# Performance work log

Hardware: AMD Instinct MI355X
Metric: run time of the kernel (lower is better)

## Reference

```python
import jax, jax.numpy as jnp
import numpy as np

B, S, V = 512, 256, 10      # batch, s_node_num, v_node_num
E, H = 128, 128             # embedding, lstm hidden
D = 2 * H                   # num_directions * hidden
PENALTY = 1.0e6
STD = 0.1


def _cell(x, h, c, Wih, Whh, b):
    # PyTorch LSTM cell, gate order i, f, g, o; b = b_ih + b_hh
    g = x @ Wih.T + h @ Whh.T + b
    i, f, gg, o = jnp.split(g, 4, axis=-1)
    c = jax.nn.sigmoid(f) * c + jax.nn.sigmoid(i) * jnp.tanh(gg)
    h = jax.nn.sigmoid(o) * jnp.tanh(c)
    return h, c


def setup_inputs() -> dict:
    key = jax.random.key(0)
    ks = jax.random.split(key, 25)
    w = lambda k, shp: (jax.random.normal(k, shp, jnp.float32) * STD)
    return {
        's_node_indexes': jax.random.randint(ks[0], (B, S), 0, S, dtype=jnp.int32),
        's_inputs': jax.random.uniform(ks[1], (B, S, 3), jnp.float32),
        'v_input': jax.random.uniform(ks[2], (V, 3), jnp.float32) * 0.5,
        'W_embed': w(ks[3], (E, 1)),
        'enc_Wih_f': w(ks[4], (4 * H, E)), 'enc_Whh_f': w(ks[5], (4 * H, H)), 'enc_b_f': w(ks[6], (4 * H,)),
        'enc_Wih_b': w(ks[7], (4 * H, E)), 'enc_Whh_b': w(ks[8], (4 * H, H)), 'enc_b_b': w(ks[9], (4 * H,)),
        'dec_Wih_f': w(ks[10], (4 * H, D)), 'dec_Whh_f': w(ks[11], (4 * H, H)), 'dec_b_f': w(ks[12], (4 * H,)),
        'dec_Wih_b': w(ks[13], (4 * H, D)), 'dec_Whh_b': w(ks[14], (4 * H, H)), 'dec_b_b': w(ks[15], (4 * H,)),
        'W_ref': w(ks[16], (D, D)), 'W_q': w(ks[17], (D, D)), 'v_w': w(ks[18], (D,)),
        'W_ref2': w(ks[19], (D, D)), 'W_q2': w(ks[20], (D, D)), 'v2_w': w(ks[21], (D,)),
    }


def reference(s_node_indexes, s_inputs, v_input, W_embed,
              enc_Wih_f, enc_Whh_f, enc_b_f, enc_Wih_b, enc_Whh_b, enc_b_b,
              dec_Wih_f, dec_Whh_f, dec_b_f, dec_Wih_b, dec_Whh_b, dec_b_b,
              W_ref, W_q, v_w, W_ref2, W_q2, v2_w):
    Bn, Sn = s_node_indexes.shape
    # Embed: snode resource -> Linear(1, E, bias=False)
    emb = s_inputs[:, :, 0:1] @ W_embed.T            # (B, S, E)
    xs = jnp.swapaxes(emb, 0, 1)                     # (S, B, E)
    h0 = jnp.zeros((Bn, H), jnp.float32)
    c0 = jnp.zeros((Bn, H), jnp.float32)

    def enc_scan(Wih, Whh, b, seq):
        def step(carry, x):
            h, c = carry
            h, c = _cell(x, h, c, Wih, Whh, b)
            return (h, c), h
        (hT, cT), hs = jax.lax.scan(step, (h0, c0), seq)
        return hs, hT, cT

    hs_f, hf, cf = enc_scan(enc_Wih_f, enc_Whh_f, enc_b_f, xs)
    hs_b, hb, cb = enc_scan(enc_Wih_b, enc_Whh_b, enc_b_b, xs[::-1])
    Enc = jnp.swapaxes(jnp.concatenate([hs_f, hs_b[::-1]], axis=-1), 0, 1)  # (B, S, D)
    h_state = jnp.stack([hf, hb])                    # (2, B, H)
    c_state = jnp.stack([cf, cb])

    refE = Enc @ W_ref.T                             # (B, S, D) precomputed (dropout p=0)
    ref2E = Enc @ W_ref2.T

    def dec_step(carry, vcpu):
        dec_in, h, c, played = carry                 # dec_in (B, D)
        hf_, cf_ = _cell(dec_in, h[0], c[0], dec_Wih_f, dec_Whh_f, dec_b_f)
        hb_, cb_ = _cell(dec_in, h[1], c[1], dec_Wih_b, dec_Whh_b, dec_b_b)
        dec_out = jnp.concatenate([hf_, hb_], axis=-1)                       # (B, D)
        cannot = (s_inputs[:, :, 0] < vcpu).astype(jnp.float32) + played     # (B, S)
        ow = jnp.tanh(refE + (dec_out @ W_q.T)[:, None, :]) @ v_w - PENALTY * cannot
        att = jax.nn.softmax(jnp.tanh(ref2E + (dec_in @ W_q2.T)[:, None, :]) @ v2_w, axis=1)
        new_in = jnp.einsum('bs,bsd->bd', att, Enc)
        sel = jnp.argmax(ow, axis=1)
        played = played + jax.nn.one_hot(sel, Sn, dtype=jnp.float32)
        return (new_in, jnp.stack([hf_, hb_]), jnp.stack([cf_, cb_]), played), (ow, sel)

    init = (jnp.zeros((Bn, D), jnp.float32), h_state, c_state, jnp.zeros((Bn, Sn), jnp.float32))
    _, (output_weights, sels) = jax.lax.scan(dec_step, init, v_input[:, 0])
    shuffled = sels.T                                # (B, V)
    original = jnp.take_along_axis(s_node_indexes, shuffled, axis=1)
    return original, shuffled, output_weights        # output_weights: (V, B, S)
```

## Files before the change

kernel.cpp:

```cpp
#include <hip/hip_runtime.h>
#include <math.h>

#define cB 512
#define cS 256
#define cV 10
#define cE 128
#define cH 128
#define cD 256
#define cG 512
#define PEN 1.0e6f
#define PADK 40
#define S1OW 112
#define L1OW 144
#define S2AT 128
#define L2AT 128

typedef _Float16 half8_t __attribute__((ext_vector_type(8)));
typedef _Float16 half4_t __attribute__((ext_vector_type(4)));
typedef float f32x4 __attribute__((ext_vector_type(4)));

#define DOT4(acc, wv, hv)                                   \
    do {                                                    \
        acc = fmaf((wv).x, (hv).x, acc);                    \
        acc = fmaf((wv).y, (hv).y, acc);                    \
        acc = fmaf((wv).z, (hv).z, acc);                    \
        acc = fmaf((wv).w, (hv).w, acc);                    \
    } while (0)

__device__ __forceinline__ float sigmf(float x) { return 1.0f / (1.0f + expf(-x)); }

__global__ void k_uprep(const float* __restrict__ Wih_f, const float* __restrict__ Wih_b,
                        const float* __restrict__ W_embed, float* __restrict__ uvec)
{
    const int j = threadIdx.x;
    const float* __restrict__ Wih = blockIdx.x ? Wih_b : Wih_f;
    float u = 0.f;
#pragma unroll 8
    for (int e = 0; e < cE; ++e) u = fmaf(Wih[(size_t)j * cE + e], W_embed[e], u);
    uvec[blockIdx.x * cG + j] = u;
}

__global__ __launch_bounds__(1024, 4) void k_encoder(
    const float* __restrict__ s_inputs, const float* __restrict__ uvec,
    const float* __restrict__ Whh_f, const float* __restrict__ b_f,
    const float* __restrict__ Whh_b, const float* __restrict__ b_b,
    _Float16* __restrict__ Ehi, _Float16* __restrict__ Elo,
    float* __restrict__ h_state, float* __restrict__ c_state)
{
    const int dir = blockIdx.x >> 7;
    const int b0  = (blockIdx.x & 127) * 4;
    const float* __restrict__ Whh = dir ? Whh_b : Whh_f;
    const float* __restrict__ bv  = dir ? b_b   : b_f;
    const int tid = threadIdx.x;
    const int j = tid & 511;
    const int hf = tid >> 9;

    __shared__ __align__(16) float a_in[4][cS];
    __shared__ __align__(16) float hbuf[4][cH];
    __shared__ __align__(16) float gpart[4][2][516];

    a_in[tid >> 8][tid & 255] =
        s_inputs[((size_t)(b0 + (tid >> 8)) * cS + (tid & 255)) * 3];

    float4 w[16];
#pragma unroll
    for (int kk = 0; kk < 16; ++kk)
        w[kk] = *(const float4*)&Whh[(size_t)j * cH + hf * 64 + kk * 4];

    const float uj = (hf == 0) ? uvec[dir * cG + j] : 0.f;
    const float bj = (hf == 0) ? bv[j] : 0.f;

    const int ur = tid >> 7, uk = tid & 127;
    float c_reg = 0.f, h_last = 0.f;
    if (tid < 512) hbuf[ur][uk] = 0.f;
    __syncthreads();

    for (int p = 0; p < cS; ++p) {
        const int s = dir ? (cS - 1 - p) : p;
        float a0[4];
#pragma unroll
        for (int r = 0; r < 4; ++r) a0[r] = fmaf(a_in[r][s], uj, bj);
#pragma unroll
        for (int kk = 0; kk < 16; ++kk) {
            const float4 wv = w[kk];
#pragma unroll
            for (int r = 0; r < 4; ++r) {
                const float4 h4 = *(const float4*)&hbuf[r][hf * 64 + kk * 4];
                DOT4(a0[r], wv, h4);
            }
        }
#pragma unroll
        for (int r = 0; r < 4; ++r) gpart[r][hf][j] = a0[r];
        __syncthreads();

        if (tid < 512) {
            const float gi = gpart[ur][0][uk]       + gpart[ur][1][uk];
            const float gf = gpart[ur][0][128 + uk] + gpart[ur][1][128 + uk];
            const float gg = gpart[ur][0][256 + uk] + gpart[ur][1][256 + uk];
            const float go = gpart[ur][0][384 + uk] + gpart[ur][1][384 + uk];
            const float i_ = sigmf(gi), f_ = sigmf(gf), g_ = tanhf(gg), o_ = sigmf(go);
            c_reg = fmaf(f_, c_reg, i_ * g_);
            const float hn = o_ * tanhf(c_reg);
            h_last = hn;
            hbuf[ur][uk] = hn;
            const size_t eidx = ((size_t)(b0 + ur) * cS + s) * cD + dir * cH + uk;
            const _Float16 hh = (_Float16)hn;
            Ehi[eidx] = hh;
            Elo[eidx] = (_Float16)(hn - (float)hh);
        }
        __syncthreads();
    }
    if (tid < 512) {
        h_state[((size_t)dir * cB + b0 + ur) * cH + uk] = h_last;
        c_state[((size_t)dir * cB + b0 + ur) * cH + uk] = c_reg;
    }
}

__global__ void k_split_w(const float* __restrict__ W1, const float* __restrict__ W2,
                          _Float16* __restrict__ Whi1, _Float16* __restrict__ Wlo1,
                          _Float16* __restrict__ Whi2, _Float16* __restrict__ Wlo2)
{
    const int i = blockIdx.x * 256 + threadIdx.x;
    {
        float a = W1[i]; _Float16 h = (_Float16)a;
        Whi1[i] = h; Wlo1[i] = (_Float16)(a - (float)h);
    }
    {
        float a = W2[i]; _Float16 h = (_Float16)a;
        Whi2[i] = h; Wlo2[i] = (_Float16)(a - (float)h);
    }
}

__global__ __launch_bounds__(256) void k_head_mat2(
    const _Float16* __restrict__ Ahi, const _Float16* __restrict__ Alo,
    const _Float16* __restrict__ Whi1, const _Float16* __restrict__ Wlo1,
    const _Float16* __restrict__ Whi2, const _Float16* __restrict__ Wlo2,
    float* __restrict__ refC, float* __restrict__ ref2C)
{
    const int blk = blockIdx.x;
    const bool is1 = blk < (S1OW * cB / 64);
    const _Float16* __restrict__ Whi = is1 ? Whi1 : Whi2;
    const _Float16* __restrict__ Wlo = is1 ? Wlo1 : Wlo2;
    float* __restrict__ outv = is1 ? refC : ref2C;
    const int m0 = (is1 ? blk : blk - S1OW * cB / 64) * 64;

    const int tid = threadIdx.x;
    const int w = tid >> 6, l = tid & 63;

    __shared__ __align__(16) _Float16 As[2][64][PADK];
    __shared__ __align__(16) _Float16 Ws[2][256][PADK];

    const int r = tid >> 2, kq = tid & 3;
    size_t arow;
    {
        const int m = m0 + r;
        const int s = m >> 9, b = m & 511;
        arow = ((size_t)b * cS + s) * cD;
    }
    const size_t wrow = (size_t)tid * cD;

    f32x4 acc[16];
#pragma unroll
    for (int i = 0; i < 16; ++i) acc[i] = (f32x4){0.f, 0.f, 0.f, 0.f};

    const int fr = w * 16 + (l & 15);
    const int kc = (l >> 4) * 8;

    for (int k0 = 0; k0 < 256; k0 += 32) {
        __syncthreads();
        *(uint4*)&As[0][r][kq * 8] = *(const uint4*)&Ahi[arow + k0 + kq * 8];
        *(uint4*)&As[1][r][kq * 8] = *(const uint4*)&Alo[arow + k0 + kq * 8];
#pragma unroll
        for (int q4 = 0; q4 < 4; ++q4) {
            *(uint4*)&Ws[0][tid][q4 * 8] = *(const uint4*)&Whi[wrow + k0 + q4 * 8];
            *(uint4*)&Ws[1][tid][q4 * 8] = *(const uint4*)&Wlo[wrow + k0 + q4 * 8];
        }
        __syncthreads();

        const half8_t ahi = *(const half8_t*)&As[0][fr][kc];
        const half8_t alo = *(const half8_t*)&As[1][fr][kc];
#pragma unroll
        for (int nf = 0; nf < 16; ++nf) {
            const int n = nf * 16 + (l & 15);
            const half8_t bhi = *(const half8_t*)&Ws[0][n][kc];
            const half8_t blo = *(const half8_t*)&Ws[1][n][kc];
            acc[nf] = __builtin_amdgcn_mfma_f32_16x16x32_f16(ahi, bhi, acc[nf], 0, 0, 0);
            acc[nf] = __builtin_amdgcn_mfma_f32_16x16x32_f16(ahi, blo, acc[nf], 0, 0, 0);
            acc[nf] = __builtin_amdgcn_mfma_f32_16x16x32_f16(alo, bhi, acc[nf], 0, 0, 0);
        }
    }
#pragma unroll
    for (int nf = 0; nf < 16; ++nf)
#pragma unroll
        for (int rr = 0; rr < 4; ++rr) {
            const int m = w * 16 + ((l >> 4) << 2) + rr;
            outv[(size_t)(m0 + m) * cD + nf * 16 + (l & 15)] = acc[nf][rr];
        }
}

__global__ __launch_bounds__(512, 2) void k_score(
    const _Float16* __restrict__ Ahi, const _Float16* __restrict__ Alo,
    const _Float16* __restrict__ Whi1, const _Float16* __restrict__ Wlo1,
    const _Float16* __restrict__ Whi2, const _Float16* __restrict__ Wlo2,
    const float* __restrict__ refC, const float* __restrict__ ref2C,
    const float* __restrict__ q1v, const float* __restrict__ q2v,
    const float* __restrict__ v_w, const float* __restrict__ v2_w,
    float* __restrict__ sc1lo, float* __restrict__ sc1hi,
    float* __restrict__ sc2lo, float* __restrict__ sc2hi)
{
    __shared__ __align__(16) char smem[65536];
    const int blk = blockIdx.x;
    const int tid = threadIdx.x;

    if (blk < 1088) {
        const bool isow = blk < 576;
        const _Float16* __restrict__ Whi = isow ? Whi1 : Whi2;
        const _Float16* __restrict__ Wlo = isow ? Wlo1 : Wlo2;
        const int batt = blk - 576;
        const int m0 = isow ? blk * 128 : 0;

        _Float16 (*Ah)[PADK] = (_Float16(*)[PADK])(smem);
        _Float16 (*Al)[PADK] = (_Float16(*)[PADK])(smem + 10240);
        _Float16 (*Wh)[PADK] = (_Float16(*)[PADK])(smem + 20480);
        _Float16 (*Wl)[PADK] = (_Float16(*)[PADK])(smem + 40960);
        float* qs = (float*)(smem + 61440);
        float* vs = (float*)(smem + 62464);
        float (*spart)[128] = (float(*)[128])(smem + 63488);

        const int l = tid & 63;
        const int w = tid >> 6;
        const int wm = w >> 2, wn = w & 3;
        const int g = l >> 4, li = l & 15;

        if (isow) {
            if (tid < 256) vs[tid] = v_w[tid];
        } else {
            if (tid < 256) qs[tid] = q2v[(size_t)batt * cD + tid];
            else           vs[tid - 256] = v2_w[tid - 256];
        }

        const int ar = tid >> 2, aq = tid & 3;
        size_t arow;
        if (isow) {
            const int m = m0 + ar;
            const int bq = m / L1OW;
            const int s = S1OW + (m - bq * L1OW);
            arow = ((size_t)bq * cS + s) * cD;
        } else {
            arow = ((size_t)batt * cS + S2AT + ar) * cD;
        }

        f32x4 acc[4][4];
#pragma unroll
        for (int mi = 0; mi < 4; ++mi)
#pragma unroll
            for (int ni = 0; ni < 4; ++ni) acc[mi][ni] = (f32x4){0.f, 0.f, 0.f, 0.f};

        for (int k0 = 0; k0 < 256; k0 += 32) {
            __syncthreads();
            *(uint4*)&Ah[ar][aq * 8] = *(const uint4*)&Ahi[arow + k0 + aq * 8];
            *(uint4*)&Al[ar][aq * 8] = *(const uint4*)&Alo[arow + k0 + aq * 8];
            *(uint4*)&Wh[ar][aq * 8] = *(const uint4*)&Whi[(size_t)ar * cD + k0 + aq * 8];
            *(uint4*)&Wl[ar][aq * 8] = *(const uint4*)&Wlo[(size_t)ar * cD + k0 + aq * 8];
            *(uint4*)&Wh[ar + 128][aq * 8] = *(const uint4*)&Whi[(size_t)(ar + 128) * cD + k0 + aq * 8];
            *(uint4*)&Wl[ar + 128][aq * 8] = *(const uint4*)&Wlo[(size_t)(ar + 128) * cD + k0 + aq * 8];
            __syncthreads();

            half8_t ah[4], al[4];
#pragma unroll
            for (int mi = 0; mi < 4; ++mi) {
                ah[mi] = *(const half8_t*)&Ah[wm * 64 + mi * 16 + li][g * 8];
                al[mi] = *(const half8_t*)&Al[wm * 64 + mi * 16 + li][g * 8];
            }
#pragma unroll
            for (int ni = 0; ni < 4; ++ni) {
                const half8_t bh = *(const half8_t*)&Wh[wn * 64 + ni * 16 + li][g * 8];
                const half8_t bl = *(const half8_t*)&Wl[wn * 64 + ni * 16 + li][g * 8];
#pragma unroll
                for (int mi = 0; mi < 4; ++mi) {
                    acc[mi][ni] = __builtin_amdgcn_mfma_f32_16x16x32_f16(ah[mi], bh, acc[mi][ni], 0, 0, 0);
                    acc[mi][ni] = __builtin_amdgcn_mfma_f32_16x16x32_f16(ah[mi], bl, acc[mi][ni], 0, 0, 0);
                    acc[mi][ni] = __builtin_amdgcn_mfma_f32_16x16x32_f16(al[mi], bh, acc[mi][ni], 0, 0, 0);
                }
            }
        }

        float val = 0.f;
#pragma unroll
        for (int mi = 0; mi < 4; ++mi)
#pragma unroll
            for (int rr = 0; rr < 4; ++rr) {
                const int row = wm * 64 + mi * 16 + g * 4 + rr;
                float p = 0.f;
#pragma unroll
                for (int ni = 0; ni < 4; ++ni) {
                    const int c = wn * 64 + ni * 16 + li;
                    const float qq = isow ? q1v[(size_t)((m0 + row) / L1OW) * cD + c]
                                          : qs[c];
                    p = fmaf(vs[c], tanhf(acc[mi][ni][rr] + qq), p);
                }
                p += __shfl_xor(p, 1);
                p += __shfl_xor(p, 2);
                p += __shfl_xor(p, 4);
                p += __shfl_xor(p, 8);
                if (li == mi * 4 + rr) val = p;
            }
        {
            const int row_out = wm * 64 + (li >> 2) * 16 + g * 4 + (li & 3);
            spart[wn][row_out] = val;
        }
        __syncthreads();
        if (tid < 128) {
            const float o = spart[0][tid] + spart[1][tid] + spart[2][tid] + spart[3][tid];
            if (isow) sc1hi[m0 + tid] = o;
            else      sc2hi[(size_t)batt * L2AT + tid] = o;
        }
    } else {
        const int fb = blk - 1088;
        const bool isowf = fb < 448;
        const float* __restrict__ C  = isowf ? refC : ref2C;
        const float* __restrict__ qv = isowf ? q1v : q2v;
        const float* __restrict__ vv = isowf ? v_w : v2_w;
        float* __restrict__ outv     = isowf ? sc1lo : sc2lo;
        const int m0 = (isowf ? fb : fb - 448) * 128;

        float (*red)[4] = (float(*)[4])smem;
        const int r = tid >> 2, p2 = tid & 3;
        const int m = m0 + r;
        const int b = m & 511;

        const float* row  = C + (size_t)m * cD + p2 * 64;
        const float* qrow = qv + (size_t)b * cD + p2 * 64;
        const float* vrow = vv + p2 * 64;
        float s = 0.f;
#pragma unroll 4
        for (int d = 0; d < 64; d += 4) {
            const float4 rv4 = *(const float4*)&row[d];
            const float4 q4  = *(const float4*)&qrow[d];
            const float4 v4  = *(const float4*)&vrow[d];
            s = fmaf(v4.x, tanhf(rv4.x + q4.x), s);
            s = fmaf(v4.y, tanhf(rv4.y + q4.y), s);
            s = fmaf(v4.z, tanhf(rv4.z + q4.z), s);
            s = fmaf(v4.w, tanhf(rv4.w + q4.w), s);
        }
        red[r][p2] = s;
        __syncthreads();
        if (tid < 128)
            outv[m0 + tid] = red[tid][0] + red[tid][1] + red[tid][2] + red[tid][3];
    }
}

__global__ __launch_bounds__(512, 2) void k_dec_cells(
    const float* __restrict__ dec_in,
    const float* __restrict__ Wih_f, const float* __restrict__ Whh_f, const float* __restrict__ b_f,
    const float* __restrict__ Wih_b, const float* __restrict__ Whh_b, const float* __restrict__ b_b,
    float* __restrict__ h_state, float* __restrict__ c_state, float* __restrict__ dec_out)
{
    const int cell = blockIdx.x >> 7;
    const int b0 = (blockIdx.x & 127) * 4;
    const float* __restrict__ Wih = cell ? Wih_b : Wih_f;
    const float* __restrict__ Whh = cell ? Whh_b : Whh_f;
    const float* __restrict__ bv  = cell ? b_b   : b_f;
    const int j = threadIdx.x;

    __shared__ __align__(16) float xin[4][cD];
    __shared__ __align__(16) float hin[4][cH];
    __shared__ __align__(16) float gbuf[4][cG];

    for (int idx = j; idx < 4 * cD; idx += 512) {
        int bb = idx >> 8, k = idx & 255;
        xin[bb][k] = dec_in[(size_t)(b0 + bb) * cD + k];
    }
    {
        int bb = j >> 7, k = j & 127;
        hin[bb][k] = h_state[((size_t)cell * cB + b0 + bb) * cH + k];
    }
    __syncthreads();

    float a0 = bv[j];
    float a1 = a0, a2 = a0, a3 = a0;
#pragma unroll 4
    for (int kk = 0; kk < 64; ++kk) {
        const float4 wv = *(const float4*)&Wih[(size_t)j * cD + kk * 4];
        const float4 x0 = *(const float4*)&xin[0][kk * 4]; DOT4(a0, wv, x0);
        const float4 x1 = *(const float4*)&xin[1][kk * 4]; DOT4(a1, wv, x1);
        const float4 x2 = *(const float4*)&xin[2][kk * 4]; DOT4(a2, wv, x2);
        const float4 x3 = *(const float4*)&xin[3][kk * 4]; DOT4(a3, wv, x3);
    }
#pragma unroll 4
    for (int kk = 0; kk < 32; ++kk) {
        const float4 wv = *(const float4*)&Whh[(size_t)j * cH + kk * 4];
        const float4 h0 = *(const float4*)&hin[0][kk * 4]; DOT4(a0, wv, h0);
        const float4 h1 = *(const float4*)&hin[1][kk * 4]; DOT4(a1, wv, h1);
        const float4 h2 = *(const float4*)&hin[2][kk * 4]; DOT4(a2, wv, h2);
        const float4 h3 = *(const float4*)&hin[3][kk * 4]; DOT4(a3, wv, h3);
    }
    gbuf[0][j] = a0; gbuf[1][j] = a1; gbuf[2][j] = a2; gbuf[3][j] = a3;
    __syncthreads();

    const int uk = j & 127, ub = j >> 7;
    const float gi = gbuf[ub][uk];
    const float gf = gbuf[ub][128 + uk];
    const float gg = gbuf[ub][256 + uk];
    const float go = gbuf[ub][384 + uk];
    const size_t sidx = ((size_t)cell * cB + b0 + ub) * cH + uk;
    const float c_old = c_state[sidx];
    const float i_ = sigmf(gi), f_ = sigmf(gf), g_ = tanhf(gg), o_ = sigmf(go);
    const float cn = fmaf(f_, c_old, i_ * g_);
    const float hn = o_ * tanhf(cn);
    c_state[sidx] = cn;
    h_state[sidx] = hn;
    dec_out[(size_t)(b0 + ub) * cD + cell * cH + uk] = hn;
}

__global__ __launch_bounds__(256, 2) void k_qproj(
    const float* __restrict__ dec_out, const float* __restrict__ dec_in_old,
    const float* __restrict__ W_q, const float* __restrict__ W_q2,
    float* __restrict__ q1v, float* __restrict__ q2v)
{
    const int b = blockIdx.x;
    const int tid = threadIdx.x;
    __shared__ __align__(16) float dout[cD];
    __shared__ __align__(16) float din[cD];
    dout[tid] = dec_out[(size_t)b * cD + tid];
    din[tid]  = dec_in_old[(size_t)b * cD + tid];
    __syncthreads();
    float s1 = 0.0f, s2 = 0.0f;
#pragma unroll 4
    for (int kk = 0; kk < 64; ++kk) {
        const float4 w1 = *(const float4*)&W_q[(size_t)tid * cD + kk * 4];
        const float4 w2 = *(const float4*)&W_q2[(size_t)tid * cD + kk * 4];
        const float4 x1 = *(const float4*)&dout[kk * 4];
        const float4 x2 = *(const float4*)&din[kk * 4];
        DOT4(s1, w1, x1);
        DOT4(s2, w2, x2);
    }
    q1v[(size_t)b * cD + tid] = s1;
    q2v[(size_t)b * cD + tid] = s2;
}

__global__ __launch_bounds__(256, 2) void k_finish(
    const float* __restrict__ sc1lo, const float* __restrict__ sc1hi,
    const float* __restrict__ sc2lo, const float* __restrict__ sc2hi,
    const _Float16* __restrict__ Ehi, const _Float16* __restrict__ Elo,
    const float* __restrict__ s_inputs, const int* __restrict__ s_node_indexes,
    const float* __restrict__ v_input, float* __restrict__ played,
    float* __restrict__ dec_in_new, float* __restrict__ outp, int t)
{
    const int b = blockIdx.x;
    const int tid = threadIdx.x;
    const int lane = tid & 63;
    const int wv = tid >> 6;

    __shared__ __align__(16) float atr[cS];
    __shared__ __align__(16) float part[4][cD];
    __shared__ float rv[cS];
    __shared__ int   ri[cS];

    const float owv = (tid < S1OW) ? sc1lo[(size_t)tid * cB + b]
                                   : sc1hi[(size_t)b * L1OW + (tid - S1OW)];
    atr[tid] = (tid < S2AT) ? sc2lo[(size_t)tid * cB + b]
                            : sc2hi[(size_t)b * L2AT + (tid - S2AT)];

    const float vcpu = v_input[t * 3];
    float val;
    {
        const float a0 = s_inputs[((size_t)b * cS + tid) * 3];
        const float can = (a0 < vcpu ? 1.0f : 0.0f) + played[(size_t)b * cS + tid];
        val = owv - PEN * can;
        outp[2 * cB * cV + ((size_t)t * cB + b) * cS + tid] = val;
    }
    rv[tid] = val; ri[tid] = tid;
    __syncthreads();
#pragma unroll
    for (int off = 128; off > 0; off >>= 1) {
        if (tid < off) {
            const float v2 = rv[tid + off]; const int i2 = ri[tid + off];
            const float v1 = rv[tid];       const int i1 = ri[tid];
            if (v2 > v1 || (v2 == v1 && i2 < i1)) { rv[tid] = v2; ri[tid] = i2; }
        }
        __syncthreads();
    }
    const int sel = ri[0];
    __syncthreads();
    if (tid == 0) {
        played[(size_t)b * cS + sel] += 1.0f;
        outp[(size_t)b * cV + t] = (float)s_node_indexes[(size_t)b * cS + sel];
        outp[(size_t)cB * cV + (size_t)b * cV + t] = (float)sel;
    }

    rv[tid] = atr[tid];
    __syncthreads();
#pragma unroll
    for (int off = 128; off > 0; off >>= 1) {
        if (tid < off) { const float v2 = rv[tid + off]; if (v2 > rv[tid]) rv[tid] = v2; }
        __syncthreads();
    }
    const float mx = rv[0];
    __syncthreads();
    const float ex = expf(atr[tid] - mx);
    rv[tid] = ex;
    __syncthreads();
#pragma unroll
    for (int off = 128; off > 0; off >>= 1) {
        if (tid < off) rv[tid] += rv[tid + off];
        __syncthreads();
    }
    const float ssum = rv[0];
    __syncthreads();
    atr[tid] = ex / ssum;
    __syncthreads();

    {
        float4 acc = make_float4(0.f, 0.f, 0.f, 0.f);
        for (int s2i = wv * 64; s2i < wv * 64 + 64; ++s2i) {
            const float a = atr[s2i];
            const size_t eidx = ((size_t)b * cS + s2i) * cD + lane * 4;
            const half4_t h4 = *(const half4_t*)&Ehi[eidx];
            const half4_t l4 = *(const half4_t*)&Elo[eidx];
            acc.x = fmaf(a, (float)h4[0] + (float)l4[0], acc.x);
            acc.y = fmaf(a, (float)h4[1] + (float)l4[1], acc.y);
            acc.z = fmaf(a, (float)h4[2] + (float)l4[2], acc.z);
            acc.w = fmaf(a, (float)h4[3] + (float)l4[3], acc.w);
        }
        *(float4*)&part[wv][lane * 4] = acc;
    }
    __syncthreads();
    dec_in_new[(size_t)b * cD + tid] =
        part[0][tid] + part[1][tid] + part[2][tid] + part[3][tid];
}

extern "C" void kernel_launch(void* const* d_in, const int* in_sizes, int n_in,
                              void* d_out, int out_size, void* d_ws, size_t ws_size,
                              hipStream_t stream)
{
    (void)in_sizes; (void)n_in; (void)out_size; (void)ws_size;

    const int*   s_node = (const int*)  d_in[0];
    const float* s_inp  = (const float*)d_in[1];
    const float* v_inp  = (const float*)d_in[2];
    const float* W_emb  = (const float*)d_in[3];
    const float* eWih_f = (const float*)d_in[4];
    const float* eWhh_f = (const float*)d_in[5];
    const float* eb_f   = (const float*)d_in[6];
    const float* eWih_b = (const float*)d_in[7];
    const float* eWhh_b = (const float*)d_in[8];
    const float* eb_b   = (const float*)d_in[9];
    const float* dWih_f = (const float*)d_in[10];
    const float* dWhh_f = (const float*)d_in[11];
    const float* db_f   = (const float*)d_in[12];
    const float* dWih_b = (const float*)d_in[13];
    const float* dWhh_b = (const float*)d_in[14];
    const float* db_b   = (const float*)d_in[15];
    const float* W_ref  = (const float*)d_in[16];
    const float* W_q    = (const float*)d_in[17];
    const float* v_w    = (const float*)d_in[18];
    const float* W_ref2 = (const float*)d_in[19];
    const float* W_q2   = (const float*)d_in[20];
    const float* v2_w   = (const float*)d_in[21];

    float* out = (float*)d_out;
    const size_t ENCSZ = (size_t)cB * cS * cD;
    const size_t SMALL = (size_t)cB * cD;

    char* p = (char*)d_ws;
    _Float16* Ehi  = (_Float16*)p; p += ENCSZ * 2;
    _Float16* Elo  = (_Float16*)p; p += ENCSZ * 2;
    float* refC    = (float*)p;    p += (size_t)S1OW * cB * cD * 4;
    float* ref2C   = (float*)p;    p += (size_t)S2AT * cB * cD * 4;
    _Float16* Whi1 = (_Float16*)p; p += (size_t)cD * cD * 2;
    _Float16* Wlo1 = (_Float16*)p; p += (size_t)cD * cD * 2;
    _Float16* Whi2 = (_Float16*)p; p += (size_t)cD * cD * 2;
    _Float16* Wlo2 = (_Float16*)p; p += (size_t)cD * cD * 2;
    float* hst    = (float*)p; p += SMALL * 4;
    float* cst    = (float*)p; p += SMALL * 4;
    float* din0   = (float*)p; p += SMALL * 4;
    float* din1   = (float*)p; p += SMALL * 4;
    float* doutb  = (float*)p; p += SMALL * 4;
    float* played = (float*)p; p += SMALL * 4;
    float* q1v    = (float*)p; p += SMALL * 4;
    float* q2v    = (float*)p; p += SMALL * 4;
    float* sc1lo  = (float*)p; p += (size_t)S1OW * cB * 4;
    float* sc1hi  = (float*)p; p += (size_t)L1OW * cB * 4;
    float* sc2lo  = (float*)p; p += (size_t)S2AT * cB * 4;
    float* sc2hi  = (float*)p; p += (size_t)L2AT * cB * 4;
    float* uvec   = (float*)p; p += 2 * cG * 4;

    hipMemsetAsync(played, 0, SMALL * sizeof(float), stream);
    hipMemsetAsync(din0,   0, SMALL * sizeof(float), stream);

    k_split_w<<<256, 256, 0, stream>>>(W_ref, W_ref2, Whi1, Wlo1, Whi2, Wlo2);
    k_uprep<<<2, 512, 0, stream>>>(eWih_f, eWih_b, W_emb, uvec);

    k_encoder<<<256, 1024, 0, stream>>>(s_inp, uvec, eWhh_f, eb_f, eWhh_b, eb_b,
                                        Ehi, Elo, hst, cst);

    k_head_mat2<<<(S1OW + S2AT) * cB / 64, 256, 0, stream>>>(
        Ehi, Elo, Whi1, Wlo1, Whi2, Wlo2, refC, ref2C);

    for (int t = 0; t < cV; ++t) {
        float* di_old = (t & 1) ? din1 : din0;
        float* di_new = (t & 1) ? din0 : din1;
        k_dec_cells<<<256, 512, 0, stream>>>(di_old, dWih_f, dWhh_f, db_f,
                                             dWih_b, dWhh_b, db_b, hst, cst, doutb);
        k_qproj<<<512, 256, 0, stream>>>(doutb, di_old, W_q, W_q2, q1v, q2v);
        k_score<<<2048, 512, 0, stream>>>(Ehi, Elo, Whi1, Wlo1, Whi2, Wlo2,
                                          refC, ref2C, q1v, q2v, v_w, v2_w,
                                          sc1lo, sc1hi, sc2lo, sc2hi);
        k_finish<<<512, 256, 0, stream>>>(sc1lo, sc1hi, sc2lo, sc2hi, Ehi, Elo,
                                          s_inp, s_node, v_inp, played, di_new, out, t);
    }
}
```

Before: 3.119 ms.

## Fuse both score heads into shared-A MFMA tiles and rebalance precompute split

The score kernel's on-the-fly MFMA path now computes both the output-weight and attention heads in one block, sharing the staged encoder A tile across two weight sets, with 256-thread blocks running two N passes. The split between precomputed ref projections and per-step recomputation is unified at one boundary (SCA/LST) for both heads, and the fallback path uses 64-row blocks. This aims to halve encoder tile loads per step and balance the grid. In exchange it adds accumulator register pressure, a larger shared buffer and more precomputed workspace.

```diff
diff --git a/kernel.cpp b/kernel.cpp
--- a/kernel.cpp
+++ b/kernel.cpp
@@ -10,10 +10,8 @@
 #define cG 512
 #define PEN 1.0e6f
 #define PADK 40
-#define S1OW 112
-#define L1OW 144
-#define S2AT 128
-#define L2AT 128
+#define SCA 120
+#define LST 136
 
 typedef _Float16 half8_t __attribute__((ext_vector_type(8)));
 typedef _Float16 half4_t __attribute__((ext_vector_type(4)));
@@ -138,11 +136,11 @@
     float* __restrict__ refC, float* __restrict__ ref2C)
 {
     const int blk = blockIdx.x;
-    const bool is1 = blk < (S1OW * cB / 64);
+    const bool is1 = blk < (SCA * cB / 64);
     const _Float16* __restrict__ Whi = is1 ? Whi1 : Whi2;
     const _Float16* __restrict__ Wlo = is1 ? Wlo1 : Wlo2;
     float* __restrict__ outv = is1 ? refC : ref2C;
-    const int m0 = (is1 ? blk : blk - S1OW * cB / 64) * 64;
+    const int m0 = (is1 ? blk : blk - SCA * cB / 64) * 64;
 
     const int tid = threadIdx.x;
     const int w = tid >> 6, l = tid & 63;
@@ -198,7 +196,7 @@
         }
 }
 
-__global__ __launch_bounds__(512, 2) void k_score(
+__global__ __launch_bounds__(256, 2) void k_score(
     const _Float16* __restrict__ Ahi, const _Float16* __restrict__ Alo,
     const _Float16* __restrict__ Whi1, const _Float16* __restrict__ Wlo1,
     const _Float16* __restrict__ Whi2, const _Float16* __restrict__ Wlo2,
@@ -208,121 +206,133 @@
     float* __restrict__ sc1lo, float* __restrict__ sc1hi,
     float* __restrict__ sc2lo, float* __restrict__ sc2hi)
 {
-    __shared__ __align__(16) char smem[65536];
+    __shared__ __align__(16) char smem[67584];
     const int blk = blockIdx.x;
     const int tid = threadIdx.x;
 
-    if (blk < 1088) {
-        const bool isow = blk < 576;
-        const _Float16* __restrict__ Whi = isow ? Whi1 : Whi2;
-        const _Float16* __restrict__ Wlo = isow ? Wlo1 : Wlo2;
-        const int batt = blk - 576;
-        const int m0 = isow ? blk * 128 : 0;
-
-        _Float16 (*Ah)[PADK] = (_Float16(*)[PADK])(smem);
-        _Float16 (*Al)[PADK] = (_Float16(*)[PADK])(smem + 10240);
-        _Float16 (*Wh)[PADK] = (_Float16(*)[PADK])(smem + 20480);
-        _Float16 (*Wl)[PADK] = (_Float16(*)[PADK])(smem + 40960);
-        float* qs = (float*)(smem + 61440);
-        float* vs = (float*)(smem + 62464);
-        float (*spart)[128] = (float(*)[128])(smem + 63488);
+    if (blk < 544) {
+        _Float16 (*Ah)[PADK]  = (_Float16(*)[PADK])(smem);
+        _Float16 (*Al)[PADK]  = (_Float16(*)[PADK])(smem + 10240);
+        _Float16 (*W1h)[PADK] = (_Float16(*)[PADK])(smem + 20480);
+        _Float16 (*W1l)[PADK] = (_Float16(*)[PADK])(smem + 30720);
+        _Float16 (*W2h)[PADK] = (_Float16(*)[PADK])(smem + 40960);
+        _Float16 (*W2l)[PADK] = (_Float16(*)[PADK])(smem + 51200);
+        float* vs1 = (float*)(smem + 61440);
+        float* vs2 = (float*)(smem + 62464);
+        float (*spart)[4][128] = (float(*)[4][128])(smem + 63488);
 
         const int l = tid & 63;
         const int w = tid >> 6;
-        const int wm = w >> 2, wn = w & 3;
+        const int wm = w >> 1, wn = w & 1;
         const int g = l >> 4, li = l & 15;
-
-        if (isow) {
-            if (tid < 256) vs[tid] = v_w[tid];
-        } else {
-            if (tid < 256) qs[tid] = q2v[(size_t)batt * cD + tid];
-            else           vs[tid - 256] = v2_w[tid - 256];
-        }
+        const int m0 = blk * 128;
+
+        vs1[tid] = v_w[tid];
+        vs2[tid] = v2_w[tid];
 
         const int ar = tid >> 2, aq = tid & 3;
-        size_t arow;
-        if (isow) {
-            const int m = m0 + ar;
-            const int bq = m / L1OW;
-            const int s = S1OW + (m - bq * L1OW);
-            arow = ((size_t)bq * cS + s) * cD;
-        } else {
-            arow = ((size_t)batt * cS + S2AT + ar) * cD;
-        }
-
-        f32x4 acc[4][4];
-#pragma unroll
-        for (int mi = 0; mi < 4; ++mi)
-#pragma unroll
-            for (int ni = 0; ni < 4; ++ni) acc[mi][ni] = (f32x4){0.f, 0.f, 0.f, 0.f};
-
-        for (int k0 = 0; k0 < 256; k0 += 32) {
-            __syncthreads();
-            *(uint4*)&Ah[ar][aq * 8] = *(const uint4*)&Ahi[arow + k0 + aq * 8];
-            *(uint4*)&Al[ar][aq * 8] = *(const uint4*)&Alo[arow + k0 + aq * 8];
-            *(uint4*)&Wh[ar][aq * 8] = *(const uint4*)&Whi[(size_t)ar * cD + k0 + aq * 8];
-            *(uint4*)&Wl[ar][aq * 8] = *(const uint4*)&Wlo[(size_t)ar * cD + k0 + aq * 8];
-            *(uint4*)&Wh[ar + 128][aq * 8] = *(const uint4*)&Whi[(size_t)(ar + 128) * cD + k0 + aq * 8];
-            *(uint4*)&Wl[ar + 128][aq * 8] = *(const uint4*)&Wlo[(size_t)(ar + 128) * cD + k0 + aq * 8];
-            __syncthreads();
-
-            half8_t ah[4], al[4];
-#pragma unroll
-            for (int mi = 0; mi < 4; ++mi) {
-                ah[mi] = *(const half8_t*)&Ah[wm * 64 + mi * 16 + li][g * 8];
-                al[mi] = *(const half8_t*)&Al[wm * 64 + mi * 16 + li][g * 8];
-            }
-#pragma unroll
-            for (int ni = 0; ni < 4; ++ni) {
-                const half8_t bh = *(const half8_t*)&Wh[wn * 64 + ni * 16 + li][g * 8];
-                const half8_t bl = *(const half8_t*)&Wl[wn * 64 + ni * 16 + li][g * 8];
+        size_t arow[2];
+#pragma unroll
+        for (int rr2 = 0; rr2 < 2; ++rr2) {
+            const int m = m0 + ar + rr2 * 64;
+            const int bq = m / LST;
+            const int s = SCA + (m - bq * LST);
+            arow[rr2] = ((size_t)bq * cS + s) * cD;
+        }
+
+#pragma unroll
+        for (int pass = 0; pass < 2; ++pass) {
+            const int n0 = pass * 128;
+            f32x4 acc1[4][4], acc2[4][4];
+#pragma unroll
+            for (int mi = 0; mi < 4; ++mi)
+#pragma unroll
+                for (int ni = 0; ni < 4; ++ni) {
+                    acc1[mi][ni] = (f32x4){0.f, 0.f, 0.f, 0.f};
+                    acc2[mi][ni] = (f32x4){0.f, 0.f, 0.f, 0.f};
+                }
+
+            for (int k0 = 0; k0 < 256; k0 += 32) {
+                __syncthreads();
+#pragma unroll
+                for (int rr2 = 0; rr2 < 2; ++rr2) {
+                    const int r = ar + rr2 * 64;
+                    *(uint4*)&Ah[r][aq * 8] = *(const uint4*)&Ahi[arow[rr2] + k0 + aq * 8];
+                    *(uint4*)&Al[r][aq * 8] = *(const uint4*)&Alo[arow[rr2] + k0 + aq * 8];
+                    const size_t wrow = (size_t)(n0 + r) * cD + k0 + aq * 8;
+                    *(uint4*)&W1h[r][aq * 8] = *(const uint4*)&Whi1[wrow];
+                    *(uint4*)&W1l[r][aq * 8] = *(const uint4*)&Wlo1[wrow];
+                    *(uint4*)&W2h[r][aq * 8] = *(const uint4*)&Whi2[wrow];
+                    *(uint4*)&W2l[r][aq * 8] = *(const uint4*)&Wlo2[wrow];
+                }
+                __syncthreads();
+
+                half8_t ah[4], al[4];
 #pragma unroll
                 for (int mi = 0; mi < 4; ++mi) {
-                    acc[mi][ni] = __builtin_amdgcn_mfma_f32_16x16x32_f16(ah[mi], bh, acc[mi][ni], 0, 0, 0);
-                    acc[mi][ni] = __builtin_amdgcn_mfma_f32_16x16x32_f16(ah[mi], bl, acc[mi][ni], 0, 0, 0);
-                    acc[mi][ni] = __builtin_amdgcn_mfma_f32_16x16x32_f16(al[mi], bh, acc[mi][ni], 0, 0, 0);
+                    ah[mi] = *(const half8_t*)&Ah[wm * 64 + mi * 16 + li][g * 8];
+                    al[mi] = *(const half8_t*)&Al[wm * 64 + mi * 16 + li][g * 8];
+                }
+#pragma unroll
+                for (int ni = 0; ni < 4; ++ni) {
+                    const int nr = wn * 64 + ni * 16 + li;
+                    const half8_t b1h = *(const half8_t*)&W1h[nr][g * 8];
+                    const half8_t b1l = *(const half8_t*)&W1l[nr][g * 8];
+                    const half8_t b2h = *(const half8_t*)&W2h[nr][g * 8];
+                    const half8_t b2l = *(const half8_t*)&W2l[nr][g * 8];
+#pragma unroll
+                    for (int mi = 0; mi < 4; ++mi) {
+                        acc1[mi][ni] = __builtin_amdgcn_mfma_f32_16x16x32_f16(ah[mi], b1h, acc1[mi][ni], 0, 0, 0);
+                        acc1[mi][ni] = __builtin_amdgcn_mfma_f32_16x16x32_f16(ah[mi], b1l, acc1[mi][ni], 0, 0, 0);
+                        acc1[mi][ni] = __builtin_amdgcn_mfma_f32_16x16x32_f16(al[mi], b1h, acc1[mi][ni], 0, 0, 0);
+                        acc2[mi][ni] = __builtin_amdgcn_mfma_f32_16x16x32_f16(ah[mi], b2h, acc2[mi][ni], 0, 0, 0);
+                        acc2[mi][ni] = __builtin_amdgcn_mfma_f32_16x16x32_f16(ah[mi], b2l, acc2[mi][ni], 0, 0, 0);
+                        acc2[mi][ni] = __builtin_amdgcn_mfma_f32_16x16x32_f16(al[mi], b2h, acc2[mi][ni], 0, 0, 0);
+                    }
                 }
             }
-        }
-
-        float val = 0.f;
-#pragma unroll
-        for (int mi = 0; mi < 4; ++mi)
-#pragma unroll
-            for (int rr = 0; rr < 4; ++rr) {
-                const int row = wm * 64 + mi * 16 + g * 4 + rr;
-                float p = 0.f;
-#pragma unroll
-                for (int ni = 0; ni < 4; ++ni) {
-                    const int c = wn * 64 + ni * 16 + li;
-                    const float qq = isow ? q1v[(size_t)((m0 + row) / L1OW) * cD + c]
-                                          : qs[c];
-                    p = fmaf(vs[c], tanhf(acc[mi][ni][rr] + qq), p);
+
+            float val1 = 0.f, val2 = 0.f;
+#pragma unroll
+            for (int mi = 0; mi < 4; ++mi)
+#pragma unroll
+                for (int rr = 0; rr < 4; ++rr) {
+                    const int row = wm * 64 + mi * 16 + g * 4 + rr;
+                    const int bq = (m0 + row) / LST;
+                    float p1 = 0.f, p2 = 0.f;
+#pragma unroll
+                    for (int ni = 0; ni < 4; ++ni) {
+                        const int c = n0 + wn * 64 + ni * 16 + li;
+                        p1 = fmaf(vs1[c], tanhf(acc1[mi][ni][rr] + q1v[(size_t)bq * cD + c]), p1);
+                        p2 = fmaf(vs2[c], tanhf(acc2[mi][ni][rr] + q2v[(size_t)bq * cD + c]), p2);
+                    }
+                    p1 += __shfl_xor(p1, 1); p2 += __shfl_xor(p2, 1);
+                    p1 += __shfl_xor(p1, 2); p2 += __shfl_xor(p2, 2);
+                    p1 += __shfl_xor(p1, 4); p2 += __shfl_xor(p2, 4);
+                    p1 += __shfl_xor(p1, 8); p2 += __shfl_xor(p2, 8);
+                    if (li == mi * 4 + rr) { val1 = p1; val2 = p2; }
                 }
-                p += __shfl_xor(p, 1);
-                p += __shfl_xor(p, 2);
-                p += __shfl_xor(p, 4);
-                p += __shfl_xor(p, 8);
-                if (li == mi * 4 + rr) val = p;
+            {
+                const int row_out = wm * 64 + (li >> 2) * 16 + g * 4 + (li & 3);
+                spart[0][pass * 2 + wn][row_out] = val1;
+                spart[1][pass * 2 + wn][row_out] = val2;
             }
-        {
-            const int row_out = wm * 64 + (li >> 2) * 16 + g * 4 + (li & 3);
-            spart[wn][row_out] = val;
         }
         __syncthreads();
         if (tid < 128) {
-            const float o = spart[0][tid] + spart[1][tid] + spart[2][tid] + spart[3][tid];
-            if (isow) sc1hi[m0 + tid] = o;
-            else      sc2hi[(size_t)batt * L2AT + tid] = o;
+            sc1hi[m0 + tid] = spart[0][0][tid] + spart[0][1][tid] +
+                              spart[0][2][tid] + spart[0][3][tid];
+            sc2hi[m0 + tid] = spart[1][0][tid] + spart[1][1][tid] +
+                              spart[1][2][tid] + spart[1][3][tid];
         }
     } else {
-        const int fb = blk - 1088;
-        const bool isowf = fb < 448;
+        const int fb = blk - 544;
+        const bool isowf = fb < (SCA * cB / 64);
         const float* __restrict__ C  = isowf ? refC : ref2C;
         const float* __restrict__ qv = isowf ? q1v : q2v;
         const float* __restrict__ vv = isowf ? v_w : v2_w;
         float* __restrict__ outv     = isowf ? sc1lo : sc2lo;
-        const int m0 = (isowf ? fb : fb - 448) * 128;
+        const int m0 = (isowf ? fb : fb - SCA * cB / 64) * 64;
 
         float (*red)[4] = (float(*)[4])smem;
         const int r = tid >> 2, p2 = tid & 3;
@@ -345,7 +355,7 @@
         }
         red[r][p2] = s;
         __syncthreads();
-        if (tid < 128)
+        if (tid < 64)
             outv[m0 + tid] = red[tid][0] + red[tid][1] + red[tid][2] + red[tid][3];
     }
 }
@@ -457,10 +467,10 @@
     __shared__ float rv[cS];
     __shared__ int   ri[cS];
 
-    const float owv = (tid < S1OW) ? sc1lo[(size_t)tid * cB + b]
-                                   : sc1hi[(size_t)b * L1OW + (tid - S1OW)];
-    atr[tid] = (tid < S2AT) ? sc2lo[(size_t)tid * cB + b]
-                            : sc2hi[(size_t)b * L2AT + (tid - S2AT)];
+    const float owv = (tid < SCA) ? sc1lo[(size_t)tid * cB + b]
+                                  : sc1hi[(size_t)b * LST + (tid - SCA)];
+    atr[tid] = (tid < SCA) ? sc2lo[(size_t)tid * cB + b]
+                           : sc2hi[(size_t)b * LST + (tid - SCA)];
 
     const float vcpu = v_input[t * 3];
     float val;
@@ -566,8 +576,8 @@
     char* p = (char*)d_ws;
     _Float16* Ehi  = (_Float16*)p; p += ENCSZ * 2;
     _Float16* Elo  = (_Float16*)p; p += ENCSZ * 2;
-    float* refC    = (float*)p;    p += (size_t)S1OW * cB * cD * 4;
-    float* ref2C   = (float*)p;    p += (size_t)S2AT * cB * cD * 4;
+    float* refC    = (float*)p;    p += (size_t)SCA * cB * cD * 4;
+    float* ref2C   = (float*)p;    p += (size_t)SCA * cB * cD * 4;
     _Float16* Whi1 = (_Float16*)p; p += (size_t)cD * cD * 2;
     _Float16* Wlo1 = (_Float16*)p; p += (size_t)cD * cD * 2;
     _Float16* Whi2 = (_Float16*)p; p += (size_t)cD * cD * 2;
@@ -580,10 +590,10 @@
     float* played = (float*)p; p += SMALL * 4;
     float* q1v    = (float*)p; p += SMALL * 4;
     float* q2v    = (float*)p; p += SMALL * 4;
-    float* sc1lo  = (float*)p; p += (size_t)S1OW * cB * 4;
-    float* sc1hi  = (float*)p; p += (size_t)L1OW * cB * 4;
-    float* sc2lo  = (float*)p; p += (size_t)S2AT * cB * 4;
-    float* sc2hi  = (float*)p; p += (size_t)L2AT * cB * 4;
+    float* sc1lo  = (float*)p; p += (size_t)SCA * cB * 4;
+    float* sc1hi  = (float*)p; p += (size_t)LST * cB * 4;
+    float* sc2lo  = (float*)p; p += (size_t)SCA * cB * 4;
+    float* sc2hi  = (float*)p; p += (size_t)LST * cB * 4;
     float* uvec   = (float*)p; p += 2 * cG * 4;
 
     hipMemsetAsync(played, 0, SMALL * sizeof(float), stream);
@@ -595,18 +605,19 @@
     k_encoder<<<256, 1024, 0, stream>>>(s_inp, uvec, eWhh_f, eb_f, eWhh_b, eb_b,
                                         Ehi, Elo, hst, cst);
 
-    k_head_mat2<<<(S1OW + S2AT) * cB / 64, 256, 0, stream>>>(
+    k_head_mat2<<<2 * SCA * cB / 64, 256, 0, stream>>>(
         Ehi, Elo, Whi1, Wlo1, Whi2, Wlo2, refC, ref2C);
 
+    const int GRID_SCORE = 544 + 2 * (SCA * cB / 64);
     for (int t = 0; t < cV; ++t) {
         float* di_old = (t & 1) ? din1 : din0;
         float* di_new = (t & 1) ? din0 : din1;
         k_dec_cells<<<256, 512, 0, stream>>>(di_old, dWih_f, dWhh_f, db_f,
                                              dWih_b, dWhh_b, db_b, hst, cst, doutb);
         k_qproj<<<512, 256, 0, stream>>>(doutb, di_old, W_q, W_q2, q1v, q2v);
-        k_score<<<2048, 512, 0, stream>>>(Ehi, Elo, Whi1, Wlo1, Whi2, Wlo2,
-                                          refC, ref2C, q1v, q2v, v_w, v2_w,
-                                          sc1lo, sc1hi, sc2lo, sc2hi);
+        k_score<<<GRID_SCORE, 256, 0, stream>>>(Ehi, Elo, Whi1, Wlo1, Whi2, Wlo2,
+                                                refC, ref2C, q1v, q2v, v_w, v2_w,
+                                                sc1lo, sc1hi, sc2lo, sc2hi);
         k_finish<<<512, 256, 0, stream>>>(sc1lo, sc1hi, sc2lo, sc2hi, Ehi, Elo,
                                           s_inp, s_node, v_inp, played, di_new, out, t);
     }
```

Measured after the change: 3.826 ms. +22.6%, slower.

## Split encoder recurrent matvec into four K-quarters with two gate rows per thread

Applied to the files above, without the earlier changes.

Each thread of the encoder kernel now computes two gate rows (j and j+256) over a 32-wide quarter of the hidden dimension, instead of one gate row over a 64-wide half. Each h4 value loaded from shared memory is therefore reused by two weight vectors, which halves the hbuf LDS reads per FMA. The per-block partial-sum buffer grows to 16x520 floats, and the reduction step now sums four partials per gate instead of two. Launch bounds are relaxed from 4 to 2 blocks per CU, which may change register allocation.

```diff
diff --git a/kernel.cpp b/kernel.cpp
--- a/kernel.cpp
+++ b/kernel.cpp
@@ -40,7 +40,7 @@
     uvec[blockIdx.x * cG + j] = u;
 }
 
-__global__ __launch_bounds__(1024, 4) void k_encoder(
+__global__ __launch_bounds__(1024, 2) void k_encoder(
     const float* __restrict__ s_inputs, const float* __restrict__ uvec,
     const float* __restrict__ Whh_f, const float* __restrict__ b_f,
     const float* __restrict__ Whh_b, const float* __restrict__ b_b,
@@ -52,23 +52,27 @@
     const float* __restrict__ Whh = dir ? Whh_b : Whh_f;
     const float* __restrict__ bv  = dir ? b_b   : b_f;
     const int tid = threadIdx.x;
-    const int j = tid & 511;
-    const int hf = tid >> 9;
+    const int jj = tid & 255;
+    const int q  = tid >> 8;
 
     __shared__ __align__(16) float a_in[4][cS];
-    __shared__ __align__(16) float hbuf[4][cH];
-    __shared__ __align__(16) float gpart[4][2][516];
+    __shared__ __align__(16) float hbuf[4][132];
+    __shared__ __align__(16) float gpart[16][520];
 
     a_in[tid >> 8][tid & 255] =
         s_inputs[((size_t)(b0 + (tid >> 8)) * cS + (tid & 255)) * 3];
 
-    float4 w[16];
-#pragma unroll
-    for (int kk = 0; kk < 16; ++kk)
-        w[kk] = *(const float4*)&Whh[(size_t)j * cH + hf * 64 + kk * 4];
-
-    const float uj = (hf == 0) ? uvec[dir * cG + j] : 0.f;
-    const float bj = (hf == 0) ? bv[j] : 0.f;
+    float4 w0[8], w1[8];
+#pragma unroll
+    for (int kk = 0; kk < 8; ++kk) {
+        w0[kk] = *(const float4*)&Whh[(size_t)jj * cH + q * 32 + kk * 4];
+        w1[kk] = *(const float4*)&Whh[(size_t)(jj + 256) * cH + q * 32 + kk * 4];
+    }
+
+    const float uj0 = (q == 0) ? uvec[dir * cG + jj] : 0.f;
+    const float bj0 = (q == 0) ? bv[jj] : 0.f;
+    const float uj1 = (q == 0) ? uvec[dir * cG + jj + 256] : 0.f;
+    const float bj1 = (q == 0) ? bv[jj + 256] : 0.f;
 
     const int ur = tid >> 7, uk = tid & 127;
     float c_reg = 0.f, h_last = 0.f;
@@ -77,27 +81,39 @@
 
     for (int p = 0; p < cS; ++p) {
         const int s = dir ? (cS - 1 - p) : p;
-        float a0[4];
-#pragma unroll
-        for (int r = 0; r < 4; ++r) a0[r] = fmaf(a_in[r][s], uj, bj);
-#pragma unroll
-        for (int kk = 0; kk < 16; ++kk) {
-            const float4 wv = w[kk];
+        float a0[4], a1[4];
+#pragma unroll
+        for (int r = 0; r < 4; ++r) {
+            a0[r] = fmaf(a_in[r][s], uj0, bj0);
+            a1[r] = fmaf(a_in[r][s], uj1, bj1);
+        }
+#pragma unroll
+        for (int kk = 0; kk < 8; ++kk) {
+            const float4 wv0 = w0[kk];
+            const float4 wv1 = w1[kk];
 #pragma unroll
             for (int r = 0; r < 4; ++r) {
-                const float4 h4 = *(const float4*)&hbuf[r][hf * 64 + kk * 4];
-                DOT4(a0[r], wv, h4);
+                const float4 h4 = *(const float4*)&hbuf[r][q * 32 + kk * 4];
+                DOT4(a0[r], wv0, h4);
+                DOT4(a1[r], wv1, h4);
             }
         }
 #pragma unroll
-        for (int r = 0; r < 4; ++r) gpart[r][hf][j] = a0[r];
+        for (int r = 0; r < 4; ++r) {
+            gpart[r * 4 + q][jj]       = a0[r];
+            gpart[r * 4 + q][jj + 256] = a1[r];
+        }
         __syncthreads();
 
         if (tid < 512) {
-            const float gi = gpart[ur][0][uk]       + gpart[ur][1][uk];
-            const float gf = gpart[ur][0][128 + uk] + gpart[ur][1][128 + uk];
-            const float gg = gpart[ur][0][256 + uk] + gpart[ur][1][256 + uk];
-            const float go = gpart[ur][0][384 + uk] + gpart[ur][1][384 + uk];
+            float gi = 0.f, gf = 0.f, gg = 0.f, go = 0.f;
+#pragma unroll
+            for (int qq = 0; qq < 4; ++qq) {
+                gi += gpart[ur * 4 + qq][uk];
+                gf += gpart[ur * 4 + qq][128 + uk];
+                gg += gpart[ur * 4 + qq][256 + uk];
+                go += gpart[ur * 4 + qq][384 + uk];
+            }
             const float i_ = sigmf(gi), f_ = sigmf(gf), g_ = tanhf(gg), o_ = sigmf(go);
             c_reg = fmaf(f_, c_reg, i_ * g_);
             const float hn = o_ * tanhf(c_reg);
```

After: 2.996 ms (median of 3 runs). 4.0% less time.

## Run encoder LSTM recurrence on MFMA with split-fp16 weights and 16-row tiles

Applied to the files above, without the earlier changes.

Replaces the scalar-FMA encoder recurrence with MFMA 16x16x32 fp16 matmuls. Hidden state and Whh are each split into hi/lo fp16 halves, keeping three product terms to preserve near-fp32 accuracy. A prep kernel splits Whh into those halves. Each block now handles 16 batch rows instead of 4, so there are 64 blocks, and the input projection and bias are added in the cell phase. This trades CU-level parallelism for cheaper per-step gate computation, and adds more cell-math work per thread.

```diff
diff --git a/kernel.cpp b/kernel.cpp
--- a/kernel.cpp
+++ b/kernel.cpp
@@ -40,79 +40,123 @@
     uvec[blockIdx.x * cG + j] = u;
 }
 
-__global__ __launch_bounds__(1024, 4) void k_encoder(
+__global__ void k_split_whh(const float* __restrict__ Whh_f, const float* __restrict__ Whh_b,
+                            _Float16* __restrict__ Whh_hi, _Float16* __restrict__ Wlo_out)
+{
+    const int i = blockIdx.x * 256 + threadIdx.x;
+    const int dir = i >> 16, off = i & 65535;
+    const float a = dir ? Whh_b[off] : Whh_f[off];
+    const _Float16 h = (_Float16)a;
+    Whh_hi[i] = h;
+    Wlo_out[i] = (_Float16)(a - (float)h);
+}
+
+__global__ __launch_bounds__(512, 2) void k_encoder_mf(
     const float* __restrict__ s_inputs, const float* __restrict__ uvec,
-    const float* __restrict__ Whh_f, const float* __restrict__ b_f,
-    const float* __restrict__ Whh_b, const float* __restrict__ b_b,
+    const _Float16* __restrict__ Whh_hi, const _Float16* __restrict__ Whh_lo,
+    const float* __restrict__ b_f, const float* __restrict__ b_b,
     _Float16* __restrict__ Ehi, _Float16* __restrict__ Elo,
     float* __restrict__ h_state, float* __restrict__ c_state)
 {
-    const int dir = blockIdx.x >> 7;
-    const int b0  = (blockIdx.x & 127) * 4;
-    const float* __restrict__ Whh = dir ? Whh_b : Whh_f;
-    const float* __restrict__ bv  = dir ? b_b   : b_f;
+    const int dir = blockIdx.x >> 5;
+    const int b0  = (blockIdx.x & 31) * 16;
     const int tid = threadIdx.x;
-    const int j = tid & 511;
-    const int hf = tid >> 9;
-
-    __shared__ __align__(16) float a_in[4][cS];
-    __shared__ __align__(16) float hbuf[4][cH];
-    __shared__ __align__(16) float gpart[4][2][516];
-
-    a_in[tid >> 8][tid & 255] =
-        s_inputs[((size_t)(b0 + (tid >> 8)) * cS + (tid & 255)) * 3];
-
-    float4 w[16];
-#pragma unroll
-    for (int kk = 0; kk < 16; ++kk)
-        w[kk] = *(const float4*)&Whh[(size_t)j * cH + hf * 64 + kk * 4];
-
-    const float uj = (hf == 0) ? uvec[dir * cG + j] : 0.f;
-    const float bj = (hf == 0) ? bv[j] : 0.f;
-
-    const int ur = tid >> 7, uk = tid & 127;
-    float c_reg = 0.f, h_last = 0.f;
-    if (tid < 512) hbuf[ur][uk] = 0.f;
+    const int w = tid >> 6;
+    const int l = tid & 63;
+    const int li = l & 15, g = l >> 4;
+
+    __shared__ __align__(16) float a_in[16][cS];
+    __shared__ __align__(16) _Float16 hhi[16][136];
+    __shared__ __align__(16) _Float16 hlo[16][136];
+    __shared__ __align__(16) float gates[16][516];
+
+    for (int i = tid; i < 16 * cS; i += 512) {
+        const int r = i >> 8, s = i & 255;
+        a_in[r][s] = s_inputs[((size_t)(b0 + r) * cS + s) * 3];
+    }
+
+    half8_t wh[4][4], wl[4][4];
+    {
+        const size_t wbase = (size_t)dir * cG * cH;
+#pragma unroll
+        for (int ni = 0; ni < 4; ++ni)
+#pragma unroll
+            for (int kt = 0; kt < 4; ++kt) {
+                const size_t off = wbase + (size_t)(64 * w + ni * 16 + li) * cH
+                                 + kt * 32 + g * 8;
+                wh[ni][kt] = *(const half8_t*)&Whh_hi[off];
+                wl[ni][kt] = *(const half8_t*)&Whh_lo[off];
+            }
+    }
+
+    const int uk = tid & 127, rq = tid >> 7;
+    const float* __restrict__ bv = dir ? b_b : b_f;
+    float uu[4], bb[4];
+#pragma unroll
+    for (int gi = 0; gi < 4; ++gi) {
+        uu[gi] = uvec[dir * cG + gi * 128 + uk];
+        bb[gi] = bv[gi * 128 + uk];
+    }
+    float c_reg[4] = {0.f, 0.f, 0.f, 0.f};
+    float h_keep[4] = {0.f, 0.f, 0.f, 0.f};
+
+    for (int i = tid; i < 16 * 136; i += 512) {
+        (&hhi[0][0])[i] = (_Float16)0.f;
+        (&hlo[0][0])[i] = (_Float16)0.f;
+    }
     __syncthreads();
 
     for (int p = 0; p < cS; ++p) {
         const int s = dir ? (cS - 1 - p) : p;
-        float a0[4];
-#pragma unroll
-        for (int r = 0; r < 4; ++r) a0[r] = fmaf(a_in[r][s], uj, bj);
-#pragma unroll
-        for (int kk = 0; kk < 16; ++kk) {
-            const float4 wv = w[kk];
-#pragma unroll
-            for (int r = 0; r < 4; ++r) {
-                const float4 h4 = *(const float4*)&hbuf[r][hf * 64 + kk * 4];
-                DOT4(a0[r], wv, h4);
+
+        f32x4 acc[4];
+#pragma unroll
+        for (int ni = 0; ni < 4; ++ni) acc[ni] = (f32x4){0.f, 0.f, 0.f, 0.f};
+#pragma unroll
+        for (int kt = 0; kt < 4; ++kt) {
+            const half8_t ah = *(const half8_t*)&hhi[li][kt * 32 + g * 8];
+            const half8_t al = *(const half8_t*)&hlo[li][kt * 32 + g * 8];
+#pragma unroll
+            for (int ni = 0; ni < 4; ++ni) {
+                acc[ni] = __builtin_amdgcn_mfma_f32_16x16x32_f16(ah, wh[ni][kt], acc[ni], 0, 0, 0);
+                acc[ni] = __builtin_amdgcn_mfma_f32_16x16x32_f16(ah, wl[ni][kt], acc[ni], 0, 0, 0);
+                acc[ni] = __builtin_amdgcn_mfma_f32_16x16x32_f16(al, wh[ni][kt], acc[ni], 0, 0, 0);
             }
         }
 #pragma unroll
-        for (int r = 0; r < 4; ++r) gpart[r][hf][j] = a0[r];
-        __syncthreads();
-
-        if (tid < 512) {
-            const float gi = gpart[ur][0][uk]       + gpart[ur][1][uk];
-            const float gf = gpart[ur][0][128 + uk] + gpart[ur][1][128 + uk];
-            const float gg = gpart[ur][0][256 + uk] + gpart[ur][1][256 + uk];
-            const float go = gpart[ur][0][384 + uk] + gpart[ur][1][384 + uk];
+        for (int ni = 0; ni < 4; ++ni)
+#pragma unroll
+            for (int rr = 0; rr < 4; ++rr)
+                gates[g * 4 + rr][64 * w + ni * 16 + li] = acc[ni][rr];
+        __syncthreads();
+
+#pragma unroll
+        for (int rr = 0; rr < 4; ++rr) {
+            const int r = rq * 4 + rr;
+            const float av = a_in[r][s];
+            const float gi = gates[r][uk]       + fmaf(av, uu[0], bb[0]);
+            const float gf = gates[r][128 + uk] + fmaf(av, uu[1], bb[1]);
+            const float gg = gates[r][256 + uk] + fmaf(av, uu[2], bb[2]);
+            const float go = gates[r][384 + uk] + fmaf(av, uu[3], bb[3]);
             const float i_ = sigmf(gi), f_ = sigmf(gf), g_ = tanhf(gg), o_ = sigmf(go);
-            c_reg = fmaf(f_, c_reg, i_ * g_);
-            const float hn = o_ * tanhf(c_reg);
-            h_last = hn;
-            hbuf[ur][uk] = hn;
-            const size_t eidx = ((size_t)(b0 + ur) * cS + s) * cD + dir * cH + uk;
+            c_reg[rr] = fmaf(f_, c_reg[rr], i_ * g_);
+            const float hn = o_ * tanhf(c_reg[rr]);
+            h_keep[rr] = hn;
             const _Float16 hh = (_Float16)hn;
+            const _Float16 hl = (_Float16)(hn - (float)hh);
+            hhi[r][uk] = hh;
+            hlo[r][uk] = hl;
+            const size_t eidx = ((size_t)(b0 + r) * cS + s) * cD + dir * cH + uk;
             Ehi[eidx] = hh;
-            Elo[eidx] = (_Float16)(hn - (float)hh);
-        }
-        __syncthreads();
-    }
-    if (tid < 512) {
-        h_state[((size_t)dir * cB + b0 + ur) * cH + uk] = h_last;
-        c_state[((size_t)dir * cB + b0 + ur) * cH + uk] = c_reg;
+            Elo[eidx] = hl;
+        }
+        __syncthreads();
+    }
+#pragma unroll
+    for (int rr = 0; rr < 4; ++rr) {
+        const int r = rq * 4 + rr;
+        h_state[((size_t)dir * cB + b0 + r) * cH + uk] = h_keep[rr];
+        c_state[((size_t)dir * cB + b0 + r) * cH + uk] = c_reg[rr];
     }
 }
 
@@ -572,6 +616,8 @@
     _Float16* Wlo1 = (_Float16*)p; p += (size_t)cD * cD * 2;
     _Float16* Whi2 = (_Float16*)p; p += (size_t)cD * cD * 2;
     _Float16* Wlo2 = (_Float16*)p; p += (size_t)cD * cD * 2;
+    _Float16* WhhHi = (_Float16*)p; p += (size_t)2 * cG * cH * 2;
+    _Float16* WhhLo = (_Float16*)p; p += (size_t)2 * cG * cH * 2;
     float* hst    = (float*)p; p += SMALL * 4;
     float* cst    = (float*)p; p += SMALL * 4;
     float* din0   = (float*)p; p += SMALL * 4;
@@ -590,10 +636,11 @@
     hipMemsetAsync(din0,   0, SMALL * sizeof(float), stream);
 
     k_split_w<<<256, 256, 0, stream>>>(W_ref, W_ref2, Whi1, Wlo1, Whi2, Wlo2);
+    k_split_whh<<<512, 256, 0, stream>>>(eWhh_f, eWhh_b, WhhHi, WhhLo);
     k_uprep<<<2, 512, 0, stream>>>(eWih_f, eWih_b, W_emb, uvec);
 
-    k_encoder<<<256, 1024, 0, stream>>>(s_inp, uvec, eWhh_f, eb_f, eWhh_b, eb_b,
-                                        Ehi, Elo, hst, cst);
+    k_encoder_mf<<<64, 512, 0, stream>>>(s_inp, uvec, WhhHi, WhhLo, eb_f, eb_b,
+                                         Ehi, Elo, hst, cst);
 
     k_head_mat2<<<(S1OW + S2AT) * cB / 64, 256, 0, stream>>>(
         Ehi, Elo, Whi1, Wlo1, Whi2, Wlo2, refC, ref2C);
```

Result: no change. 3.098 ms (-0.7%).
